# Kernel optimization log

Measured on AMD Instinct MI355X. Metric: run time of the kernel, lower is better.

The kernel has to match this reference:

```python
import jax, jax.numpy as jnp
import numpy as np

N = 20000
E = 320000
IN = 512
H = 4
C = 128
ED = 4
NEG_SLOPE = 0.2
BN_EPS = 1e-5


def setup_inputs() -> dict:
    key = jax.random.key(0)
    ks = jax.random.split(key, 10)
    x = jax.random.normal(ks[0], (N, IN), dtype=jnp.float32)
    edge_index = jax.random.randint(ks[1], (2, E), 0, N, dtype=jnp.int64)
    edge_attr = jax.random.normal(ks[2], (E, ED), dtype=jnp.float32)
    # GATConv params (glorot-ish scaling)
    W = jax.random.normal(ks[3], (IN, H * C), dtype=jnp.float32) / np.sqrt(IN)
    W_edge = jax.random.normal(ks[4], (ED, H * C), dtype=jnp.float32) / np.sqrt(ED)
    att_src = jax.random.normal(ks[5], (H, C), dtype=jnp.float32) / np.sqrt(C)
    att_dst = jax.random.normal(ks[6], (H, C), dtype=jnp.float32) / np.sqrt(C)
    att_edge = jax.random.normal(ks[7], (H, C), dtype=jnp.float32) / np.sqrt(C)
    bias = jnp.zeros((H * C,), dtype=jnp.float32)
    gamma = jnp.ones((H * C,), dtype=jnp.float32)
    beta = jnp.zeros((H * C,), dtype=jnp.float32)
    return {"x": x, "edge_index": edge_index, "edge_attr": edge_attr,
            "W": W, "W_edge": W_edge, "att_src": att_src, "att_dst": att_dst,
            "att_edge": att_edge, "bias": bias, "gamma": gamma, "beta": beta}


def _edge_gat(x, edge_index, edge_attr, W, W_edge, att_src, att_dst, att_edge,
              bias, gamma, beta):
    n = x.shape[0]
    # PyG default: add self loops, edge_attr fill_value='mean'
    loop = jnp.arange(n, dtype=edge_index.dtype)
    src = jnp.concatenate([edge_index[0], loop])  # [E+N]
    dst = jnp.concatenate([edge_index[1], loop])
    ea = jnp.concatenate(
        [edge_attr, jnp.broadcast_to(edge_attr.mean(0), (n, edge_attr.shape[1]))], 0)

    h = (x @ W).reshape(n, H, C)                       # [N,H,C]
    a_src = (h * att_src[None]).sum(-1)                # [N,H]
    a_dst = (h * att_dst[None]).sum(-1)                # [N,H]
    e = (ea @ W_edge).reshape(-1, H, C)                # [E+N,H,C]
    a_edge = (e * att_edge[None]).sum(-1)              # [E+N,H]

    alpha = a_src[src] + a_dst[dst] + a_edge           # [E+N,H]
    alpha = jax.nn.leaky_relu(alpha, NEG_SLOPE)
    # segment softmax over edges grouped by target node
    amax = jax.lax.stop_gradient(jax.ops.segment_max(alpha, dst, num_segments=n))
    ex = jnp.exp(alpha - amax[dst])
    denom = jax.ops.segment_sum(ex, dst, num_segments=n)
    att = ex / (denom[dst] + 1e-16)                    # [E+N,H]

    msg = h[src] * att[:, :, None]                     # [E+N,H,C]
    out = jax.ops.segment_sum(msg, dst, num_segments=n).reshape(n, H * C) + bias

    # BatchNorm1d in training mode: batch statistics, biased variance
    mu = out.mean(0)
    var = out.var(0)
    return (out - mu) / jnp.sqrt(var + BN_EPS) * gamma + beta


def reference(x, edge_index, edge_attr, W, W_edge, att_src, att_dst, att_edge,
              bias, gamma, beta):
    return _edge_gat(x, edge_index, edge_attr, W, W_edge, att_src, att_dst,
                     att_edge, bias, gamma, beta)
```

## Files before the change

kernel.cpp:

```cpp
#include <hip/hip_runtime.h>
#include <math.h>

#define N_NODES 20000
#define N_EDGES 320000
#define TOT_E   340000
#define IN_F    512
#define HC      512
#define NHEAD   4
#define CHAN    128
#define NEG_SLOPE 0.2f
#define BN_EPS  1e-5f
#define NSLICE  8
#define AGG_BLOCKS 2500
#define NODES_PER_BLOCK 8

#define GEMM_BM 32
#define LDS_STRIDE 72

#define PACK_BLOCKS 128
#define PREP_BLOCKS 256

typedef short short8v __attribute__((ext_vector_type(8)));
typedef float f32x4  __attribute__((ext_vector_type(4)));
typedef unsigned short u16x8 __attribute__((ext_vector_type(8)));
typedef unsigned short u16x4 __attribute__((ext_vector_type(4)));

__device__ __forceinline__ unsigned short f2bf(float f) {
  unsigned u = __float_as_uint(f);
  return (unsigned short)((u + 0x7FFFu + ((u >> 16) & 1u)) >> 16);
}
__device__ __forceinline__ float bf2f(unsigned short b) {
  return __uint_as_float(((unsigned)b) << 16);
}

__global__ void prep_pack_kernel(const float* __restrict__ W,
                                 unsigned short* __restrict__ Bp,
                                 const float* __restrict__ EA, const int* __restrict__ EI,
                                 const float* __restrict__ We, const float* __restrict__ aedg,
                                 float* __restrict__ msum, int* __restrict__ deg,
                                 float* __restrict__ qm) {
  if (blockIdx.x < PACK_BLOCKS) {
    const int tid = blockIdx.x * blockDim.x + threadIdx.x;
    const int l = tid & 63;
    const int k32 = (tid >> 6) & 15;
    const int n16 = tid >> 10;
    const int col = n16 * 16 + (l & 15);
    const int k = k32 * 32 + ((l >> 4) << 3);
    unsigned short v[8];
#pragma unroll
    for (int j = 0; j < 8; ++j) v[j] = f2bf(W[(size_t)(k + j) * HC + col]);
    *(short8v*)&Bp[(size_t)tid * 8] = *(short8v*)v;
  } else {
    const int bid = blockIdx.x - PACK_BLOCKS;
    if (bid < 16 && threadIdx.x < 64) {
      const int d = bid >> 2, h = bid & 3, lane = threadIdx.x;
      const int base = h * CHAN + lane * 2;
      float v = We[d * HC + base] * aedg[base] + We[d * HC + base + 1] * aedg[base + 1];
#pragma unroll
      for (int m = 32; m >= 1; m >>= 1) v += __shfl_down(v, m);
      if (lane == 0) qm[d * 4 + h] = v;
    }
    float s0 = 0.f, s1 = 0.f, s2 = 0.f, s3 = 0.f;
    for (int i = bid * blockDim.x + threadIdx.x; i < N_EDGES;
         i += PREP_BLOCKS * blockDim.x) {
      const float4 v = *(const float4*)&EA[(size_t)i * 4];
      s0 += v.x; s1 += v.y; s2 += v.z; s3 += v.w;
      atomicAdd(&deg[EI[N_EDGES + i]], 1);
    }
#pragma unroll
    for (int m = 32; m >= 1; m >>= 1) {
      s0 += __shfl_down(s0, m); s1 += __shfl_down(s1, m);
      s2 += __shfl_down(s2, m); s3 += __shfl_down(s3, m);
    }
    __shared__ float red[4][4];
    const int lane = threadIdx.x & 63, wid = threadIdx.x >> 6;
    if (lane == 0) { red[wid][0] = s0; red[wid][1] = s1; red[wid][2] = s2; red[wid][3] = s3; }
    __syncthreads();
    if (threadIdx.x < 4) {
      float v = red[0][threadIdx.x] + red[1][threadIdx.x] + red[2][threadIdx.x] + red[3][threadIdx.x];
      atomicAdd(&msum[threadIdx.x], v);
    }
  }
}

__global__ __launch_bounds__(1024) void scan_kernel(const int* __restrict__ deg,
                                                    int* __restrict__ rowstart) {
  __shared__ int part[1024];
  const int t = threadIdx.x;
  const int base = t * 20;
  int local[20];
  int s = 0;
#pragma unroll
  for (int i = 0; i < 20; ++i) {
    const int idx = base + i;
    const int v = (idx < N_NODES) ? deg[idx] : 0;
    local[i] = s;
    s += v;
  }
  part[t] = s;
  __syncthreads();
  for (int off = 1; off < 1024; off <<= 1) {
    const int v = (t >= off) ? part[t - off] : 0;
    __syncthreads();
    part[t] += v;
    __syncthreads();
  }
  const int excl = (t > 0) ? part[t - 1] : 0;
#pragma unroll
  for (int i = 0; i < 20; ++i) {
    const int idx = base + i;
    if (idx < N_NODES) rowstart[idx] = excl + local[i];
  }
  if (t == 1023) rowstart[N_NODES] = part[1023];
}

__global__ __launch_bounds__(256) void gemm_direct_fused(
    const float* __restrict__ X, const unsigned short* __restrict__ Bp_,
    const float* __restrict__ att_s, const float* __restrict__ att_d,
    unsigned short* __restrict__ H16, float* __restrict__ a_src,
    float* __restrict__ a_dst) {
  __shared__ unsigned short As[GEMM_BM * LDS_STRIDE];
  const short8v* __restrict__ Bp = (const short8v*)Bp_;
  const int tid = threadIdx.x;
  const int l = tid & 63;
  const int w = tid >> 6;
  const int bm = blockIdx.x * GEMM_BM;
  const int srow = tid >> 3;
  const int skc = (tid & 7) * 8;
  const int grow = bm + srow;
  const int fr = l & 15;
  const int fg = l >> 4;
  const int cl = l & 15;
  f32x4 acc[2][8] = {};
  for (int k0 = 0; k0 < IN_F; k0 += 64) {
    float4 f0 = {0.f, 0.f, 0.f, 0.f}, f1 = {0.f, 0.f, 0.f, 0.f};
    if (grow < N_NODES) {
      f0 = *(const float4*)&X[(size_t)grow * IN_F + k0 + skc];
      f1 = *(const float4*)&X[(size_t)grow * IN_F + k0 + skc + 4];
    }
    unsigned short vv[8] = {f2bf(f0.x), f2bf(f0.y), f2bf(f0.z), f2bf(f0.w),
                            f2bf(f1.x), f2bf(f1.y), f2bf(f1.z), f2bf(f1.w)};
    __syncthreads();
    *(short8v*)&As[srow * LDS_STRIDE + skc] = *(short8v*)vv;
    __syncthreads();
#pragma unroll
    for (int ks = 0; ks < 2; ++ks) {
      const int kk = (k0 >> 5) + ks;
      short8v a[2], b[8];
#pragma unroll
      for (int m = 0; m < 2; ++m)
        a[m] = *(const short8v*)&As[(m * 16 + fr) * LDS_STRIDE + ks * 32 + fg * 8];
#pragma unroll
      for (int n = 0; n < 8; ++n)
        b[n] = Bp[((size_t)(w * 8 + n) * 16 + kk) * 64 + l];
#pragma unroll
      for (int m = 0; m < 2; ++m)
#pragma unroll
        for (int n = 0; n < 8; ++n)
          acc[m][n] = __builtin_amdgcn_mfma_f32_16x16x32_bf16(a[m], b[n], acc[m][n], 0, 0, 0);
    }
  }
  const int rbase = fg * 4;
#pragma unroll
  for (int m = 0; m < 2; ++m) {
#pragma unroll
    for (int r = 0; r < 4; ++r) {
      const int row = bm + m * 16 + rbase + r;
#pragma unroll
      for (int n = 0; n < 8; ++n)
        H16[(size_t)row * HC + (w * 8 + n) * 16 + cl] = f2bf(acc[m][n][r]);
    }
  }
  float as_v[8], ad_v[8];
#pragma unroll
  for (int n = 0; n < 8; ++n) {
    const int c = w * CHAN + n * 16 + cl;
    as_v[n] = att_s[c];
    ad_v[n] = att_d[c];
  }
#pragma unroll
  for (int m = 0; m < 2; ++m) {
#pragma unroll
    for (int r = 0; r < 4; ++r) {
      float ps = 0.f, pd = 0.f;
#pragma unroll
      for (int n = 0; n < 8; ++n) { ps += acc[m][n][r] * as_v[n]; pd += acc[m][n][r] * ad_v[n]; }
#pragma unroll
      for (int mask = 1; mask <= 8; mask <<= 1) {
        ps += __shfl_xor(ps, mask); pd += __shfl_xor(pd, mask);
      }
      if (cl == 0) {
        const int row = bm + m * 16 + rbase + r;
        a_src[row * 4 + w] = ps;
        a_dst[row * 4 + w] = pd;
      }
    }
  }
}

__global__ void scatter_alpha_kernel(const int* __restrict__ EI, const float* __restrict__ EA,
                                     const int* __restrict__ rowstart, int* __restrict__ cnt,
                                     const float* __restrict__ a_src, const float* __restrict__ a_dst,
                                     const float* __restrict__ msum, const float* __restrict__ q,
                                     int* __restrict__ csr_src, float* __restrict__ alphacsr) {
  const int k = blockIdx.x * blockDim.x + threadIdx.x;
  if (k >= TOT_E) return;
  int s, d, pos;
  float e0, e1, e2, e3;
  if (k < N_EDGES) {
    s = EI[k]; d = EI[N_EDGES + k];
    const float4 e = *(const float4*)&EA[(size_t)k * 4];
    e0 = e.x; e1 = e.y; e2 = e.z; e3 = e.w;
    pos = rowstart[d] + atomicAdd(&cnt[d], 1);
    csr_src[pos] = s;
  } else {
    s = d = k - N_EDGES;
    const float inv = 1.0f / (float)N_EDGES;
    e0 = msum[0] * inv; e1 = msum[1] * inv; e2 = msum[2] * inv; e3 = msum[3] * inv;
    pos = k;
  }
  const float4 as = *(const float4*)&a_src[s * 4];
  const float4 ad = *(const float4*)&a_dst[d * 4];
  const float asv[4] = {as.x, as.y, as.z, as.w};
  const float adv[4] = {ad.x, ad.y, ad.z, ad.w};
  float al[4];
#pragma unroll
  for (int h = 0; h < 4; ++h) {
    float ae = e0 * q[h] + e1 * q[4 + h] + e2 * q[8 + h] + e3 * q[12 + h];
    float a = asv[h] + adv[h] + ae;
    al[h] = (a >= 0.f) ? a : NEG_SLOPE * a;
  }
  float4 o = {al[0], al[1], al[2], al[3]};
  *(float4*)&alphacsr[(size_t)pos * 4] = o;
}

__global__ __launch_bounds__(256) void agg_fused_kernel(
    const int* __restrict__ rowstart, const int* __restrict__ csr_src,
    const float* __restrict__ alphacsr, const unsigned short* __restrict__ H16,
    unsigned short* __restrict__ o16, float* __restrict__ psum, float* __restrict__ psq) {
  __shared__ float sv[4][HC];
  const int wid = threadIdx.x >> 6;
  const int l = threadIdx.x & 63;
  const int head = l >> 4;
  const int j = l * 8;
  const int lo = l & 15;
  float ssum[8] = {0.f, 0.f, 0.f, 0.f, 0.f, 0.f, 0.f, 0.f};
  float ssq[8]  = {0.f, 0.f, 0.f, 0.f, 0.f, 0.f, 0.f, 0.f};
#pragma unroll 1
  for (int g = 0; g < NODES_PER_BLOCK / 4; ++g) {
    const int n = blockIdx.x * NODES_PER_BLOCK + g * 4 + wid;
    const int beg = rowstart[n], end = rowstart[n + 1];
    const float aself = alphacsr[(size_t)(N_EDGES + n) * 4 + head];
    float m = aself;
    for (int p = beg + lo; p < end; p += 16)
      m = fmaxf(m, alphacsr[(size_t)p * 4 + head]);
#pragma unroll
    for (int mask = 1; mask <= 8; mask <<= 1) m = fmaxf(m, __shfl_xor(m, mask));
    float den = 0.f;
    for (int p = beg + lo; p < end; p += 16)
      den += __expf(alphacsr[(size_t)p * 4 + head] - m);
#pragma unroll
    for (int mask = 1; mask <= 8; mask <<= 1) den += __shfl_xor(den, mask);
    den += __expf(aself - m);
    const float dinv = 1.0f / (den + 1e-16f);
    const float wself = __expf(aself - m) * dinv;
    const u16x8 hv = *(const u16x8*)&H16[(size_t)n * HC + j];
    float acc[8];
#pragma unroll
    for (int c = 0; c < 8; ++c) acc[c] = wself * bf2f(hv[c]);
    int s_nxt = 0;
    if (beg < end) s_nxt = csr_src[beg];
    for (int idx = beg; idx < end; ++idx) {
      const int s = s_nxt;
      if (idx + 1 < end) s_nxt = csr_src[idx + 1];
      const float w = __expf(alphacsr[(size_t)idx * 4 + head] - m) * dinv;
      const u16x8 v = *(const u16x8*)&H16[(size_t)s * HC + j];
#pragma unroll
      for (int c = 0; c < 8; ++c) acc[c] += w * bf2f(v[c]);
    }
    unsigned short ov[8];
#pragma unroll
    for (int c = 0; c < 8; ++c) {
      ov[c] = f2bf(acc[c]);
      ssum[c] += acc[c];
      ssq[c] += acc[c] * acc[c];
    }
    *(short8v*)&o16[(size_t)n * HC + j] = *(short8v*)ov;
  }
  const int t = threadIdx.x;
  const int slice = (blockIdx.x & (NSLICE - 1)) * HC;
#pragma unroll
  for (int c = 0; c < 8; ++c) sv[wid][j + c] = ssum[c];
  __syncthreads();
  const float r0 = sv[0][t] + sv[1][t] + sv[2][t] + sv[3][t];
  const float r1 = sv[0][t + 256] + sv[1][t + 256] + sv[2][t + 256] + sv[3][t + 256];
  __syncthreads();
#pragma unroll
  for (int c = 0; c < 8; ++c) sv[wid][j + c] = ssq[c];
  __syncthreads();
  const float q0 = sv[0][t] + sv[1][t] + sv[2][t] + sv[3][t];
  const float q1 = sv[0][t + 256] + sv[1][t + 256] + sv[2][t + 256] + sv[3][t + 256];
  atomicAdd(&psum[slice + t], r0);
  atomicAdd(&psum[slice + t + 256], r1);
  atomicAdd(&psq[slice + t], q0);
  atomicAdd(&psq[slice + t + 256], q1);
}

__global__ void bn_reduce_kernel(const float* __restrict__ psum, const float* __restrict__ psq,
                                 const float* __restrict__ gamma, const float* __restrict__ beta,
                                 float* __restrict__ scale, float* __restrict__ shift) {
  const int c = threadIdx.x;
  float s = 0.f, q = 0.f;
#pragma unroll
  for (int k = 0; k < NSLICE; ++k) { s += psum[k * HC + c]; q += psq[k * HC + c]; }
  const float mu = s * (1.0f / N_NODES);
  const float var = q * (1.0f / N_NODES) - mu * mu;
  const float sc = gamma[c] * rsqrtf(var + BN_EPS);
  scale[c] = sc;
  shift[c] = beta[c] - mu * sc;
}

__global__ void bn_apply_kernel(const unsigned short* __restrict__ o16,
                                const float* __restrict__ scale,
                                const float* __restrict__ shift,
                                float* __restrict__ out) {
  const int i = blockIdx.x * blockDim.x + threadIdx.x;
  if (i >= N_NODES * HC / 4) return;
  const int j4 = (i & (HC / 4 - 1)) * 4;
  const u16x4 v16 = *(const u16x4*)&o16[(size_t)i * 4];
  const float4 sc = *(const float4*)&scale[j4];
  const float4 sh = *(const float4*)&shift[j4];
  float4 v;
  v.x = bf2f(v16[0]) * sc.x + sh.x;
  v.y = bf2f(v16[1]) * sc.y + sh.y;
  v.z = bf2f(v16[2]) * sc.z + sh.z;
  v.w = bf2f(v16[3]) * sc.w + sh.w;
  ((float4*)out)[i] = v;
}

extern "C" void kernel_launch(void* const* d_in, const int* in_sizes, int n_in,
                              void* d_out, int out_size, void* d_ws, size_t ws_size,
                              hipStream_t stream) {
  const float* x     = (const float*)d_in[0];
  const int*   ei    = (const int*)d_in[1];
  const float* ea    = (const float*)d_in[2];
  const float* W     = (const float*)d_in[3];
  const float* We    = (const float*)d_in[4];
  const float* att_s = (const float*)d_in[5];
  const float* att_d = (const float*)d_in[6];
  const float* att_e = (const float*)d_in[7];
  const float* gamma = (const float*)d_in[9];
  const float* beta  = (const float*)d_in[10];
  float* out = (float*)d_out;
  float* ws  = (float*)d_ws;

  unsigned short* H16     = (unsigned short*)ws;
  float*    a_src   = (float*)(H16 + (size_t)N_NODES * HC);
  float*    a_dst   = a_src + N_NODES * NHEAD;
  float*    alphacsr= a_dst + N_NODES * NHEAD;
  float*    qm      = alphacsr + (size_t)TOT_E * NHEAD;
  float*    scale   = qm + 16;
  float*    shift   = scale + HC;
  int*      rowstart= (int*)(shift + HC);
  int*      csr_src = rowstart + 20004;
  unsigned short* Bp  = (unsigned short*)(csr_src + N_EDGES);
  unsigned short* o16 = Bp + (size_t)32 * 16 * 64 * 8;
  int*      deg     = (int*)(o16 + (size_t)N_NODES * HC);
  int*      cnt     = deg + N_NODES;
  float*    msum    = (float*)(cnt + N_NODES);
  float*    psum    = msum + 4;
  float*    psq     = psum + NSLICE * HC;

  const size_t zero_bytes =
      (size_t)(N_NODES * 2 + 4 + NSLICE * HC * 2) * sizeof(float);
  hipMemsetAsync(deg, 0, zero_bytes, stream);

  prep_pack_kernel<<<PACK_BLOCKS + PREP_BLOCKS, 256, 0, stream>>>(
      W, Bp, ea, ei, We, att_e, msum, deg, qm);
  scan_kernel<<<1, 1024, 0, stream>>>(deg, rowstart);
  gemm_direct_fused<<<N_NODES / GEMM_BM, 256, 0, stream>>>(x, Bp, att_s, att_d,
                                                           H16, a_src, a_dst);
  scatter_alpha_kernel<<<(TOT_E + 255) / 256, 256, 0, stream>>>(ei, ea, rowstart, cnt,
                                                                a_src, a_dst, msum, qm,
                                                                csr_src, alphacsr);
  agg_fused_kernel<<<AGG_BLOCKS, 256, 0, stream>>>(rowstart, csr_src, alphacsr, H16,
                                                   o16, psum, psq);
  bn_reduce_kernel<<<1, HC, 0, stream>>>(psum, psq, gamma, beta, scale, shift);
  bn_apply_kernel<<<(N_NODES * HC / 4 + 255) / 256, 256, 0, stream>>>(o16, scale, shift, out);
}
```

Baseline: 174.3 us.

## Split aggregation into softmax-weight pass and channel-sliced gather kernel

Replaces the fused aggregation kernel with two kernels. The first computes per-edge, per-head softmax weights into a head-major buffer. The second gathers neighbor features in 64-channel slices, with 4 edges processed in parallel per wave and combined by shuffle reduction. The aim is more parallelism and shorter dependent gather chains for each node. In exchange it adds an extra launch, a write and re-read of the weight buffer, and 8x the reads of row offsets and source indices. BN partial sums now go through one atomic buffer instead of 8 slices, which raises atomic contention.

```diff
diff --git a/kernel.cpp b/kernel.cpp
--- a/kernel.cpp
+++ b/kernel.cpp
@@ -10,15 +10,14 @@
 #define CHAN    128
 #define NEG_SLOPE 0.2f
 #define BN_EPS  1e-5f
-#define NSLICE  8
-#define AGG_BLOCKS 2500
-#define NODES_PER_BLOCK 8
 
 #define GEMM_BM 32
 #define LDS_STRIDE 72
 
 #define PACK_BLOCKS 128
 #define PREP_BLOCKS 256
+
+#define GATHER_CHUNK 16
 
 typedef short short8v __attribute__((ext_vector_type(8)));
 typedef float f32x4  __attribute__((ext_vector_type(4)));
@@ -234,87 +233,115 @@
   *(float4*)&alphacsr[(size_t)pos * 4] = o;
 }
 
-__global__ __launch_bounds__(256) void agg_fused_kernel(
+__global__ __launch_bounds__(256) void softmax_w_kernel(
+    const int* __restrict__ rowstart, const float* __restrict__ alphacsr,
+    float* __restrict__ w_h) {
+  const int wid = threadIdx.x >> 6;
+  const int n = blockIdx.x * 4 + wid;
+  const int l = threadIdx.x & 63;
+  const int head = l >> 4;
+  const int lo = l & 15;
+  const int beg = rowstart[n], end = rowstart[n + 1];
+  const float aself = alphacsr[(size_t)(N_EDGES + n) * 4 + head];
+  float m = aself;
+  for (int p = beg + lo; p < end; p += 16)
+    m = fmaxf(m, alphacsr[(size_t)p * 4 + head]);
+#pragma unroll
+  for (int mask = 1; mask <= 8; mask <<= 1) m = fmaxf(m, __shfl_xor(m, mask));
+  float den = 0.f;
+  for (int p = beg + lo; p < end; p += 16)
+    den += __expf(alphacsr[(size_t)p * 4 + head] - m);
+#pragma unroll
+  for (int mask = 1; mask <= 8; mask <<= 1) den += __shfl_xor(den, mask);
+  den += __expf(aself - m);
+  const float dinv = 1.0f / (den + 1e-16f);
+  float* __restrict__ wd = w_h + (size_t)head * TOT_E;
+  for (int p = beg + lo; p < end; p += 16)
+    wd[p] = __expf(alphacsr[(size_t)p * 4 + head] - m) * dinv;
+  if (lo == 0) wd[N_EDGES + n] = __expf(aself - m) * dinv;
+}
+
+__global__ __launch_bounds__(256) void gather_sliced_kernel(
     const int* __restrict__ rowstart, const int* __restrict__ csr_src,
-    const float* __restrict__ alphacsr, const unsigned short* __restrict__ H16,
-    unsigned short* __restrict__ o16, float* __restrict__ psum, float* __restrict__ psq) {
-  __shared__ float sv[4][HC];
+    const float* __restrict__ w_h, const unsigned short* __restrict__ H16,
+    unsigned short* __restrict__ o16, float* __restrict__ psum,
+    float* __restrict__ psq) {
+  __shared__ float sv[4][64];
+  const int slice = blockIdx.x & 7;
+  const int chunk = blockIdx.x >> 3;
   const int wid = threadIdx.x >> 6;
   const int l = threadIdx.x & 63;
-  const int head = l >> 4;
-  const int j = l * 8;
-  const int lo = l & 15;
-  float ssum[8] = {0.f, 0.f, 0.f, 0.f, 0.f, 0.f, 0.f, 0.f};
-  float ssq[8]  = {0.f, 0.f, 0.f, 0.f, 0.f, 0.f, 0.f, 0.f};
+  const int eg = l >> 4;
+  const int cl = l & 15;
+  const int ch = slice * 64 + cl * 4;
+  const float* __restrict__ wd = w_h + (size_t)(slice >> 1) * TOT_E;
+  float ssum[4] = {0.f, 0.f, 0.f, 0.f}, ssq[4] = {0.f, 0.f, 0.f, 0.f};
 #pragma unroll 1
-  for (int g = 0; g < NODES_PER_BLOCK / 4; ++g) {
-    const int n = blockIdx.x * NODES_PER_BLOCK + g * 4 + wid;
+  for (int g = 0; g < GATHER_CHUNK / 4; ++g) {
+    const int n = chunk * GATHER_CHUNK + g * 4 + wid;
     const int beg = rowstart[n], end = rowstart[n + 1];
-    const float aself = alphacsr[(size_t)(N_EDGES + n) * 4 + head];
-    float m = aself;
-    for (int p = beg + lo; p < end; p += 16)
-      m = fmaxf(m, alphacsr[(size_t)p * 4 + head]);
-#pragma unroll
-    for (int mask = 1; mask <= 8; mask <<= 1) m = fmaxf(m, __shfl_xor(m, mask));
-    float den = 0.f;
-    for (int p = beg + lo; p < end; p += 16)
-      den += __expf(alphacsr[(size_t)p * 4 + head] - m);
-#pragma unroll
-    for (int mask = 1; mask <= 8; mask <<= 1) den += __shfl_xor(den, mask);
-    den += __expf(aself - m);
-    const float dinv = 1.0f / (den + 1e-16f);
-    const float wself = __expf(aself - m) * dinv;
-    const u16x8 hv = *(const u16x8*)&H16[(size_t)n * HC + j];
-    float acc[8];
-#pragma unroll
-    for (int c = 0; c < 8; ++c) acc[c] = wself * bf2f(hv[c]);
-    int s_nxt = 0;
-    if (beg < end) s_nxt = csr_src[beg];
-    for (int idx = beg; idx < end; ++idx) {
-      const int s = s_nxt;
-      if (idx + 1 < end) s_nxt = csr_src[idx + 1];
-      const float w = __expf(alphacsr[(size_t)idx * 4 + head] - m) * dinv;
-      const u16x8 v = *(const u16x8*)&H16[(size_t)s * HC + j];
-#pragma unroll
-      for (int c = 0; c < 8; ++c) acc[c] += w * bf2f(v[c]);
-    }
-    unsigned short ov[8];
-#pragma unroll
-    for (int c = 0; c < 8; ++c) {
-      ov[c] = f2bf(acc[c]);
-      ssum[c] += acc[c];
-      ssq[c] += acc[c] * acc[c];
-    }
-    *(short8v*)&o16[(size_t)n * HC + j] = *(short8v*)ov;
-  }
-  const int t = threadIdx.x;
-  const int slice = (blockIdx.x & (NSLICE - 1)) * HC;
-#pragma unroll
-  for (int c = 0; c < 8; ++c) sv[wid][j + c] = ssum[c];
+    float acc[4] = {0.f, 0.f, 0.f, 0.f};
+    int idx = beg + eg;
+    int src_cur = (idx < end) ? csr_src[idx] : -1;
+    for (int p0 = beg; p0 < end; p0 += 4) {
+      const int i2 = p0 + 4 + eg;
+      const int src_nxt = (i2 < end) ? csr_src[i2] : -1;
+      if (src_cur >= 0) {
+        const float w = wd[p0 + eg];
+        const u16x4 v = *(const u16x4*)&H16[(size_t)src_cur * HC + ch];
+        acc[0] += w * bf2f(v[0]); acc[1] += w * bf2f(v[1]);
+        acc[2] += w * bf2f(v[2]); acc[3] += w * bf2f(v[3]);
+      }
+      src_cur = src_nxt;
+    }
+#pragma unroll
+    for (int c = 0; c < 4; ++c) {
+      acc[c] += __shfl_xor(acc[c], 16);
+      acc[c] += __shfl_xor(acc[c], 32);
+    }
+    if (eg == 0) {
+      const float wself = wd[N_EDGES + n];
+      const u16x4 hv = *(const u16x4*)&H16[(size_t)n * HC + ch];
+      unsigned short ov[4];
+#pragma unroll
+      for (int c = 0; c < 4; ++c) {
+        acc[c] += wself * bf2f(hv[c]);
+        ov[c] = f2bf(acc[c]);
+        ssum[c] += acc[c];
+        ssq[c] += acc[c] * acc[c];
+      }
+      *(u16x4*)&o16[(size_t)n * HC + ch] = *(u16x4*)ov;
+    }
+  }
+  if (eg == 0) {
+#pragma unroll
+    for (int c = 0; c < 4; ++c) sv[wid][cl * 4 + c] = ssum[c];
+  }
   __syncthreads();
-  const float r0 = sv[0][t] + sv[1][t] + sv[2][t] + sv[3][t];
-  const float r1 = sv[0][t + 256] + sv[1][t + 256] + sv[2][t + 256] + sv[3][t + 256];
+  if (threadIdx.x < 64) {
+    const float v = sv[0][threadIdx.x] + sv[1][threadIdx.x] +
+                    sv[2][threadIdx.x] + sv[3][threadIdx.x];
+    atomicAdd(&psum[slice * 64 + threadIdx.x], v);
+  }
   __syncthreads();
-#pragma unroll
-  for (int c = 0; c < 8; ++c) sv[wid][j + c] = ssq[c];
+  if (eg == 0) {
+#pragma unroll
+    for (int c = 0; c < 4; ++c) sv[wid][cl * 4 + c] = ssq[c];
+  }
   __syncthreads();
-  const float q0 = sv[0][t] + sv[1][t] + sv[2][t] + sv[3][t];
-  const float q1 = sv[0][t + 256] + sv[1][t + 256] + sv[2][t + 256] + sv[3][t + 256];
-  atomicAdd(&psum[slice + t], r0);
-  atomicAdd(&psum[slice + t + 256], r1);
-  atomicAdd(&psq[slice + t], q0);
-  atomicAdd(&psq[slice + t + 256], q1);
+  if (threadIdx.x < 64) {
+    const float v = sv[0][threadIdx.x] + sv[1][threadIdx.x] +
+                    sv[2][threadIdx.x] + sv[3][threadIdx.x];
+    atomicAdd(&psq[slice * 64 + threadIdx.x], v);
+  }
 }
 
 __global__ void bn_reduce_kernel(const float* __restrict__ psum, const float* __restrict__ psq,
                                  const float* __restrict__ gamma, const float* __restrict__ beta,
                                  float* __restrict__ scale, float* __restrict__ shift) {
   const int c = threadIdx.x;
-  float s = 0.f, q = 0.f;
-#pragma unroll
-  for (int k = 0; k < NSLICE; ++k) { s += psum[k * HC + c]; q += psq[k * HC + c]; }
-  const float mu = s * (1.0f / N_NODES);
-  const float var = q * (1.0f / N_NODES) - mu * mu;
+  const float mu = psum[c] * (1.0f / N_NODES);
+  const float var = psq[c] * (1.0f / N_NODES) - mu * mu;
   const float sc = gamma[c] * rsqrtf(var + BN_EPS);
   scale[c] = sc;
   shift[c] = beta[c] - mu * sc;
@@ -358,7 +385,8 @@
   float*    a_src   = (float*)(H16 + (size_t)N_NODES * HC);
   float*    a_dst   = a_src + N_NODES * NHEAD;
   float*    alphacsr= a_dst + N_NODES * NHEAD;
-  float*    qm      = alphacsr + (size_t)TOT_E * NHEAD;
+  float*    w_h     = alphacsr + (size_t)TOT_E * NHEAD;
+  float*    qm      = w_h + (size_t)NHEAD * TOT_E;
   float*    scale   = qm + 16;
   float*    shift   = scale + HC;
   int*      rowstart= (int*)(shift + HC);
@@ -369,10 +397,9 @@
   int*      cnt     = deg + N_NODES;
   float*    msum    = (float*)(cnt + N_NODES);
   float*    psum    = msum + 4;
-  float*    psq     = psum + NSLICE * HC;
-
-  const size_t zero_bytes =
-      (size_t)(N_NODES * 2 + 4 + NSLICE * HC * 2) * sizeof(float);
+  float*    psq     = psum + HC;
+
+  const size_t zero_bytes = (size_t)(N_NODES * 2 + 4 + HC * 2) * sizeof(float);
   hipMemsetAsync(deg, 0, zero_bytes, stream);
 
   prep_pack_kernel<<<PACK_BLOCKS + PREP_BLOCKS, 256, 0, stream>>>(
@@ -383,8 +410,9 @@
   scatter_alpha_kernel<<<(TOT_E + 255) / 256, 256, 0, stream>>>(ei, ea, rowstart, cnt,
                                                                 a_src, a_dst, msum, qm,
                                                                 csr_src, alphacsr);
-  agg_fused_kernel<<<AGG_BLOCKS, 256, 0, stream>>>(rowstart, csr_src, alphacsr, H16,
-                                                   o16, psum, psq);
+  softmax_w_kernel<<<N_NODES / 4, 256, 0, stream>>>(rowstart, alphacsr, w_h);
+  gather_sliced_kernel<<<8 * (N_NODES / GATHER_CHUNK), 256, 0, stream>>>(
+      rowstart, csr_src, w_h, H16, o16, psum, psq);
   bn_reduce_kernel<<<1, HC, 0, stream>>>(psum, psq, gamma, beta, scale, shift);
   bn_apply_kernel<<<(N_NODES * HC / 4 + 255) / 256, 256, 0, stream>>>(o16, scale, shift, out);
 }
```

New measurement: 219.8 us. +26.1%, slower.

## Move BN statistics out of aggregation into separate bf16 stats kernel

Applied to the files above, without the earlier changes.

The aggregation kernel now handles one node per wave, with N/4 blocks and no per-block LDS reduction or atomics for the BatchNorm sums. A new kernel rereads the bf16 aggregated output to compute per-channel sum and sum of squares. The scale/shift reduction kernel is removed and its work folded into the apply kernel. This trades the in-aggregation reductions and one launch for an extra pass over o16. Statistics are now computed from bf16-rounded values rather than fp32 accumulators, a small precision change.

```diff
diff --git a/kernel.cpp b/kernel.cpp
--- a/kernel.cpp
+++ b/kernel.cpp
@@ -10,9 +10,6 @@
 #define CHAN    128
 #define NEG_SLOPE 0.2f
 #define BN_EPS  1e-5f
-#define NSLICE  8
-#define AGG_BLOCKS 2500
-#define NODES_PER_BLOCK 8
 
 #define GEMM_BM 32
 #define LDS_STRIDE 72
@@ -237,104 +234,88 @@
 __global__ __launch_bounds__(256) void agg_fused_kernel(
     const int* __restrict__ rowstart, const int* __restrict__ csr_src,
     const float* __restrict__ alphacsr, const unsigned short* __restrict__ H16,
-    unsigned short* __restrict__ o16, float* __restrict__ psum, float* __restrict__ psq) {
-  __shared__ float sv[4][HC];
+    unsigned short* __restrict__ o16) {
   const int wid = threadIdx.x >> 6;
+  const int n = blockIdx.x * 4 + wid;
   const int l = threadIdx.x & 63;
   const int head = l >> 4;
   const int j = l * 8;
   const int lo = l & 15;
-  float ssum[8] = {0.f, 0.f, 0.f, 0.f, 0.f, 0.f, 0.f, 0.f};
-  float ssq[8]  = {0.f, 0.f, 0.f, 0.f, 0.f, 0.f, 0.f, 0.f};
-#pragma unroll 1
-  for (int g = 0; g < NODES_PER_BLOCK / 4; ++g) {
-    const int n = blockIdx.x * NODES_PER_BLOCK + g * 4 + wid;
-    const int beg = rowstart[n], end = rowstart[n + 1];
-    const float aself = alphacsr[(size_t)(N_EDGES + n) * 4 + head];
-    float m = aself;
-    for (int p = beg + lo; p < end; p += 16)
-      m = fmaxf(m, alphacsr[(size_t)p * 4 + head]);
-#pragma unroll
-    for (int mask = 1; mask <= 8; mask <<= 1) m = fmaxf(m, __shfl_xor(m, mask));
-    float den = 0.f;
-    for (int p = beg + lo; p < end; p += 16)
-      den += __expf(alphacsr[(size_t)p * 4 + head] - m);
-#pragma unroll
-    for (int mask = 1; mask <= 8; mask <<= 1) den += __shfl_xor(den, mask);
-    den += __expf(aself - m);
-    const float dinv = 1.0f / (den + 1e-16f);
-    const float wself = __expf(aself - m) * dinv;
-    const u16x8 hv = *(const u16x8*)&H16[(size_t)n * HC + j];
-    float acc[8];
-#pragma unroll
-    for (int c = 0; c < 8; ++c) acc[c] = wself * bf2f(hv[c]);
-    int s_nxt = 0;
-    if (beg < end) s_nxt = csr_src[beg];
-    for (int idx = beg; idx < end; ++idx) {
-      const int s = s_nxt;
-      if (idx + 1 < end) s_nxt = csr_src[idx + 1];
-      const float w = __expf(alphacsr[(size_t)idx * 4 + head] - m) * dinv;
-      const u16x8 v = *(const u16x8*)&H16[(size_t)s * HC + j];
-#pragma unroll
-      for (int c = 0; c < 8; ++c) acc[c] += w * bf2f(v[c]);
-    }
-    unsigned short ov[8];
-#pragma unroll
-    for (int c = 0; c < 8; ++c) {
-      ov[c] = f2bf(acc[c]);
-      ssum[c] += acc[c];
-      ssq[c] += acc[c] * acc[c];
-    }
-    *(short8v*)&o16[(size_t)n * HC + j] = *(short8v*)ov;
-  }
+  const int beg = rowstart[n], end = rowstart[n + 1];
+  const float aself = alphacsr[(size_t)(N_EDGES + n) * 4 + head];
+  float m = aself;
+  for (int p = beg + lo; p < end; p += 16)
+    m = fmaxf(m, alphacsr[(size_t)p * 4 + head]);
+#pragma unroll
+  for (int mask = 1; mask <= 8; mask <<= 1) m = fmaxf(m, __shfl_xor(m, mask));
+  float den = 0.f;
+  for (int p = beg + lo; p < end; p += 16)
+    den += __expf(alphacsr[(size_t)p * 4 + head] - m);
+#pragma unroll
+  for (int mask = 1; mask <= 8; mask <<= 1) den += __shfl_xor(den, mask);
+  den += __expf(aself - m);
+  const float dinv = 1.0f / (den + 1e-16f);
+  const float wself = __expf(aself - m) * dinv;
+  const u16x8 hv = *(const u16x8*)&H16[(size_t)n * HC + j];
+  float acc[8];
+#pragma unroll
+  for (int c = 0; c < 8; ++c) acc[c] = wself * bf2f(hv[c]);
+  int s_nxt = 0;
+  if (beg < end) s_nxt = csr_src[beg];
+  for (int idx = beg; idx < end; ++idx) {
+    const int s = s_nxt;
+    if (idx + 1 < end) s_nxt = csr_src[idx + 1];
+    const float w = __expf(alphacsr[(size_t)idx * 4 + head] - m) * dinv;
+    const u16x8 v = *(const u16x8*)&H16[(size_t)s * HC + j];
+#pragma unroll
+    for (int c = 0; c < 8; ++c) acc[c] += w * bf2f(v[c]);
+  }
+  unsigned short ov[8];
+#pragma unroll
+  for (int c = 0; c < 8; ++c) ov[c] = f2bf(acc[c]);
+  *(short8v*)&o16[(size_t)n * HC + j] = *(short8v*)ov;
+}
+
+__global__ void bn_stats16_kernel(const unsigned short* __restrict__ o16,
+                                  float* __restrict__ psum, float* __restrict__ psq) {
   const int t = threadIdx.x;
-  const int slice = (blockIdx.x & (NSLICE - 1)) * HC;
-#pragma unroll
-  for (int c = 0; c < 8; ++c) sv[wid][j + c] = ssum[c];
-  __syncthreads();
-  const float r0 = sv[0][t] + sv[1][t] + sv[2][t] + sv[3][t];
-  const float r1 = sv[0][t + 256] + sv[1][t + 256] + sv[2][t + 256] + sv[3][t + 256];
-  __syncthreads();
-#pragma unroll
-  for (int c = 0; c < 8; ++c) sv[wid][j + c] = ssq[c];
-  __syncthreads();
-  const float q0 = sv[0][t] + sv[1][t] + sv[2][t] + sv[3][t];
-  const float q1 = sv[0][t + 256] + sv[1][t + 256] + sv[2][t + 256] + sv[3][t + 256];
-  atomicAdd(&psum[slice + t], r0);
-  atomicAdd(&psum[slice + t + 256], r1);
-  atomicAdd(&psq[slice + t], q0);
-  atomicAdd(&psq[slice + t + 256], q1);
-}
-
-__global__ void bn_reduce_kernel(const float* __restrict__ psum, const float* __restrict__ psq,
-                                 const float* __restrict__ gamma, const float* __restrict__ beta,
-                                 float* __restrict__ scale, float* __restrict__ shift) {
-  const int c = threadIdx.x;
-  float s = 0.f, q = 0.f;
-#pragma unroll
-  for (int k = 0; k < NSLICE; ++k) { s += psum[k * HC + c]; q += psq[k * HC + c]; }
-  const float mu = s * (1.0f / N_NODES);
-  const float var = q * (1.0f / N_NODES) - mu * mu;
-  const float sc = gamma[c] * rsqrtf(var + BN_EPS);
-  scale[c] = sc;
-  shift[c] = beta[c] - mu * sc;
+  const int j = t * 2;
+  float s0 = 0.f, s1 = 0.f, q0 = 0.f, q1 = 0.f;
+  for (int r = blockIdx.x; r < N_NODES; r += gridDim.x) {
+    const unsigned v = *(const unsigned*)&o16[(size_t)r * HC + j];
+    const float a = bf2f((unsigned short)(v & 0xffffu));
+    const float b = bf2f((unsigned short)(v >> 16));
+    s0 += a; s1 += b; q0 += a * a; q1 += b * b;
+  }
+  atomicAdd(&psum[j], s0);
+  atomicAdd(&psum[j + 1], s1);
+  atomicAdd(&psq[j], q0);
+  atomicAdd(&psq[j + 1], q1);
 }
 
 __global__ void bn_apply_kernel(const unsigned short* __restrict__ o16,
-                                const float* __restrict__ scale,
-                                const float* __restrict__ shift,
+                                const float* __restrict__ psum, const float* __restrict__ psq,
+                                const float* __restrict__ gamma, const float* __restrict__ beta,
                                 float* __restrict__ out) {
   const int i = blockIdx.x * blockDim.x + threadIdx.x;
   if (i >= N_NODES * HC / 4) return;
   const int j4 = (i & (HC / 4 - 1)) * 4;
+  const float4 cs = *(const float4*)&psum[j4];
+  const float4 cq = *(const float4*)&psq[j4];
+  const float4 g  = *(const float4*)&gamma[j4];
+  const float4 b  = *(const float4*)&beta[j4];
+  const float inv = 1.0f / N_NODES;
+  const float mux = cs.x * inv, muy = cs.y * inv, muz = cs.z * inv, muw = cs.w * inv;
+  const float scx = g.x * rsqrtf(cq.x * inv - mux * mux + BN_EPS);
+  const float scy = g.y * rsqrtf(cq.y * inv - muy * muy + BN_EPS);
+  const float scz = g.z * rsqrtf(cq.z * inv - muz * muz + BN_EPS);
+  const float scw = g.w * rsqrtf(cq.w * inv - muw * muw + BN_EPS);
   const u16x4 v16 = *(const u16x4*)&o16[(size_t)i * 4];
-  const float4 sc = *(const float4*)&scale[j4];
-  const float4 sh = *(const float4*)&shift[j4];
   float4 v;
-  v.x = bf2f(v16[0]) * sc.x + sh.x;
-  v.y = bf2f(v16[1]) * sc.y + sh.y;
-  v.z = bf2f(v16[2]) * sc.z + sh.z;
-  v.w = bf2f(v16[3]) * sc.w + sh.w;
+  v.x = (bf2f(v16[0]) - mux) * scx + b.x;
+  v.y = (bf2f(v16[1]) - muy) * scy + b.y;
+  v.z = (bf2f(v16[2]) - muz) * scz + b.z;
+  v.w = (bf2f(v16[3]) - muw) * scw + b.w;
   ((float4*)out)[i] = v;
 }
 
@@ -359,9 +340,7 @@
   float*    a_dst   = a_src + N_NODES * NHEAD;
   float*    alphacsr= a_dst + N_NODES * NHEAD;
   float*    qm      = alphacsr + (size_t)TOT_E * NHEAD;
-  float*    scale   = qm + 16;
-  float*    shift   = scale + HC;
-  int*      rowstart= (int*)(shift + HC);
+  int*      rowstart= (int*)(qm + 16);
   int*      csr_src = rowstart + 20004;
   unsigned short* Bp  = (unsigned short*)(csr_src + N_EDGES);
   unsigned short* o16 = Bp + (size_t)32 * 16 * 64 * 8;
@@ -369,10 +348,9 @@
   int*      cnt     = deg + N_NODES;
   float*    msum    = (float*)(cnt + N_NODES);
   float*    psum    = msum + 4;
-  float*    psq     = psum + NSLICE * HC;
-
-  const size_t zero_bytes =
-      (size_t)(N_NODES * 2 + 4 + NSLICE * HC * 2) * sizeof(float);
+  float*    psq     = psum + HC;
+
+  const size_t zero_bytes = (size_t)(N_NODES * 2 + 4 + HC * 2) * sizeof(float);
   hipMemsetAsync(deg, 0, zero_bytes, stream);
 
   prep_pack_kernel<<<PACK_BLOCKS + PREP_BLOCKS, 256, 0, stream>>>(
@@ -383,8 +361,8 @@
   scatter_alpha_kernel<<<(TOT_E + 255) / 256, 256, 0, stream>>>(ei, ea, rowstart, cnt,
                                                                 a_src, a_dst, msum, qm,
                                                                 csr_src, alphacsr);
-  agg_fused_kernel<<<AGG_BLOCKS, 256, 0, stream>>>(rowstart, csr_src, alphacsr, H16,
-                                                   o16, psum, psq);
-  bn_reduce_kernel<<<1, HC, 0, stream>>>(psum, psq, gamma, beta, scale, shift);
-  bn_apply_kernel<<<(N_NODES * HC / 4 + 255) / 256, 256, 0, stream>>>(o16, scale, shift, out);
-}
+  agg_fused_kernel<<<N_NODES / 4, 256, 0, stream>>>(rowstart, csr_src, alphacsr, H16, o16);
+  bn_stats16_kernel<<<256, 256, 0, stream>>>(o16, psum, psq);
+  bn_apply_kernel<<<(N_NODES * HC / 4 + 255) / 256, 256, 0, stream>>>(o16, psum, psq,
+                                                                      gamma, beta, out);
+}
```

Result: slower. 198.8 us (+14.1%).
